# Kernel optimization log

Measured on AMD Instinct MI355X. Metric: run time of the kernel, lower is better.

The kernel has to match this reference:

```python
import jax, jax.numpy as jnp
import numpy as np

HEAD_SIZE = 64

def setup_inputs() -> dict:
    key = jax.random.key(0)
    k1, k2, k3, k4 = jax.random.split(key, 4)
    B, T, D = 4, 4096, 768
    x = jax.random.normal(k1, (B, T, D), dtype=jnp.float32)
    Wq = jax.random.normal(k2, (D, HEAD_SIZE), dtype=jnp.float32) * (1.0 / np.sqrt(D))
    Wk = jax.random.normal(k3, (D, HEAD_SIZE), dtype=jnp.float32) * (1.0 / np.sqrt(D))
    Wv = jax.random.normal(k4, (D, HEAD_SIZE), dtype=jnp.float32) * (1.0 / np.sqrt(D))
    return {"x": x, "Wq": Wq, "Wk": Wk, "Wv": Wv}

def reference(x, Wq, Wk, Wv):
    # q,k,v: [B, T, H]
    q = jnp.einsum('btd,dh->bth', x, Wq)
    k = jnp.einsum('btd,dh->bth', x, Wk)
    v = jnp.einsum('btd,dh->bth', x, Wv)
    # scores: [B, T, T]; causal mask via lower-triangular band, -inf elsewhere
    scores = jnp.einsum('bqh,bkh->bqk', q, k)
    T = x.shape[1]
    causal = jnp.tril(jnp.ones((T, T), dtype=bool))  # band_part(ones, -1, 0)
    scores = jnp.where(causal[None, :, :], scores, -jnp.inf)
    attn = jax.nn.softmax(scores / np.sqrt(HEAD_SIZE), axis=-1)
    # dropout is identity in eval mode
    return jnp.einsum('bqk,bkh->bqh', attn, v)
```

## Files before the change

kernel.cpp:

```cpp
#include <hip/hip_runtime.h>
#include <math.h>

typedef __attribute__((ext_vector_type(8))) short short8;
typedef __attribute__((ext_vector_type(4))) float f32x4;
typedef unsigned short ushort_t;

#define TSEQ   4096
#define NBATCH 4
#define DMODEL 768
#define HS     64
#define KSPLIT 4

static __device__ __forceinline__ ushort_t f2bf(float f) {
  union { float f; unsigned u; } v; v.f = f;
  unsigned r = v.u + 0x7fffu + ((v.u >> 16) & 1u);
  return (ushort_t)(r >> 16);
}
static __device__ __forceinline__ float bf2f(ushort_t u) {
  union { unsigned u; float f; } v; v.u = ((unsigned)u) << 16; return v.f;
}

#define MFMA16(a,b,c) __builtin_amdgcn_mfma_f32_16x16x32_bf16((a),(b),(c),0,0,0)

__global__ __launch_bounds__(256) void wprep(
    const float* __restrict__ Wq, const float* __restrict__ Wk,
    const float* __restrict__ Wv, ushort_t* __restrict__ Wt)
{
  __shared__ float lds[64 * 65];
  const int m = blockIdx.x / 12, kc = blockIdx.x % 12, k0 = kc * 64;
  const float* W = (m == 0) ? Wq : (m == 1) ? Wk : Wv;
  const int tid = threadIdx.x;
#pragma unroll
  for (int i = 0; i < 16; i++) {
    const int row = i * 4 + (tid >> 6), col = tid & 63;
    lds[row * 65 + col] = W[(size_t)(k0 + row) * HS + col];
  }
  __syncthreads();
#pragma unroll
  for (int i = 0; i < 16; i++) {
    const int n = i * 4 + (tid >> 6), kk = tid & 63;
    Wt[(size_t)(m * 64 + n) * DMODEL + k0 + kk] = f2bf(lds[kk * 65 + n]);
  }
}

#define XPITCH 772
__global__ __launch_bounds__(256, 3) void qkv_mfma(
    const float* __restrict__ x, const ushort_t* __restrict__ Wt,
    ushort_t* __restrict__ q, ushort_t* __restrict__ kO, ushort_t* __restrict__ vT)
{
  __shared__ __align__(16) float xp[16 * XPITCH];

  const int tid  = threadIdx.x;
  const int ns   = tid >> 6;
  const int lane = tid & 63;
  const int l16  = lane & 15, quad = lane >> 4;
  const int M0   = blockIdx.x * 16;

  {
    const int row0 = ns * 4;
#pragma unroll
    for (int r = 0; r < 4; r++) {
      const float* gsrc = x + (size_t)(M0 + row0 + r) * DMODEL;
      float*       ldst = xp + (row0 + r) * XPITCH;
#pragma unroll
      for (int c = 0; c < 3; c++) {
        __builtin_amdgcn_global_load_lds(
            (const __attribute__((address_space(1))) float*)(gsrc + c * 256 + lane * 4),
            (__attribute__((address_space(3))) float*)(ldst + c * 256),
            16, 0, 0);
      }
    }
  }

  const ushort_t* wb = Wt + (size_t)(ns * 48 + l16) * DMODEL + quad * 8;
  short8 bp[6];
#pragma unroll
  for (int nt = 0; nt < 3; nt++)
#pragma unroll
    for (int kc = 0; kc < 2; kc++)
      bp[nt * 2 + kc] = *(const short8*)(wb + (size_t)nt * 16 * DMODEL + kc * 32);

  f32x4 acc[3];
#pragma unroll
  for (int nt = 0; nt < 3; nt++) acc[nt] = (f32x4){0.f, 0.f, 0.f, 0.f};

  __syncthreads();

  for (int ks = 0; ks < DMODEL / 64; ks++) {
    short8 bc[6];
#pragma unroll
    for (int t = 0; t < 6; t++) bc[t] = bp[t];
    if (ks < DMODEL / 64 - 1) {
#pragma unroll
      for (int nt = 0; nt < 3; nt++)
#pragma unroll
        for (int kc = 0; kc < 2; kc++)
          bp[nt * 2 + kc] =
              *(const short8*)(wb + (size_t)nt * 16 * DMODEL + (ks + 1) * 64 + kc * 32);
    }
#pragma unroll
    for (int kc = 0; kc < 2; kc++) {
      const float* ar = xp + l16 * XPITCH + ks * 64 + kc * 32 + quad * 8;
      const float4 f0 = *(const float4*)(ar);
      const float4 f1 = *(const float4*)(ar + 4);
      short8 af;
      af[0] = f2bf(f0.x); af[1] = f2bf(f0.y); af[2] = f2bf(f0.z); af[3] = f2bf(f0.w);
      af[4] = f2bf(f1.x); af[5] = f2bf(f1.y); af[6] = f2bf(f1.z); af[7] = f2bf(f1.w);
#pragma unroll
      for (int nt = 0; nt < 3; nt++)
        acc[nt] = MFMA16(af, bc[nt * 2 + kc], acc[nt]);
    }
  }

#pragma unroll
  for (int nt = 0; nt < 3; nt++) {
    const int gnt = ns * 3 + nt;
    const int mat = gnt >> 2;
    const int col = (gnt & 3) * 16 + l16;
    if (mat == 0) {
#pragma unroll
      for (int r = 0; r < 4; r++)
        q[(size_t)(M0 + quad * 4 + r) * HS + col] = f2bf(acc[nt][r] * 0.125f);
    } else if (mat == 1) {
#pragma unroll
      for (int r = 0; r < 4; r++)
        kO[(size_t)(M0 + quad * 4 + r) * HS + col] = f2bf(acc[nt][r]);
    }
  }
  __syncthreads();
  float* vls = xp;
#pragma unroll
  for (int nt = 0; nt < 3; nt++) {
    const int gnt = ns * 3 + nt;
    if ((gnt >> 2) == 2) {
      const int col = (gnt & 3) * 16 + l16;
#pragma unroll
      for (int r = 0; r < 4; r++)
        vls[(quad * 4 + r) * 65 + col] = acc[nt][r];
    }
  }
  __syncthreads();
  if (tid < 128) {
    const int d = tid >> 1, seg = tid & 1;
    short8 pk;
#pragma unroll
    for (int i = 0; i < 8; i++) pk[i] = (short)f2bf(vls[(seg * 8 + i) * 65 + d]);
    *(short8*)(vT + ((size_t)(M0 >> 12) * HS + d) * TSEQ + (M0 & (TSEQ - 1)) + seg * 8) = pk;
  }
}

#define KP 72
__global__ __launch_bounds__(128) void attn_part(
    const ushort_t* __restrict__ q, const ushort_t* __restrict__ k,
    const ushort_t* __restrict__ vT, float* __restrict__ ML, ushort_t* __restrict__ OP)
{
  __shared__ __align__(16) ushort_t sK[64 * KP];
  __shared__ __align__(16) ushort_t sV[64 * KP];
  __shared__ __align__(16) ushort_t sP[2][16 * KP];

  const int idx  = blockIdx.x;
  const int s    = idx & 3;
  const int b    = (idx >> 2) & 3;
  const int jt   = 127 - (idx >> 4);
  const int tid  = threadIdx.x;
  const int w    = tid >> 6;
  const int lane = tid & 63;
  const int l16  = lane & 15, quad = lane >> 4;
  const int R0   = jt * 32 + w * 16;

  const ushort_t* qg = q  + (size_t)b * TSEQ * HS;
  const ushort_t* kg = k  + (size_t)b * TSEQ * HS;
  const ushort_t* vg = vT + (size_t)b * HS * TSEQ;

  const short8 qf0 = *(const short8*)(qg + (R0 + l16) * HS +      quad * 8);
  const short8 qf1 = *(const short8*)(qg + (R0 + l16) * HS + 32 + quad * 8);

  f32x4 o[4];
#pragma unroll
  for (int dt = 0; dt < 4; dt++) o[dt] = (f32x4){0.f, 0.f, 0.f, 0.f};
  float mrow = -INFINITY, lrow = 0.f;

  const int nkt = jt / 2 + 1;
  short8 kpre[4], vpre[4];
  int kt = s;
  if (kt < nkt) {
    const int k0 = kt * 64;
#pragma unroll
    for (int i = 0; i < 4; i++) {
      const int c = i * 128 + tid, key = c >> 3, ch = c & 7;
      kpre[i] = *(const short8*)(kg + (size_t)(k0 + key) * HS + ch * 8);
      vpre[i] = *(const short8*)(vg + (size_t)key * TSEQ + k0 + ch * 8);
    }
  }
  for (; kt < nkt; kt += KSPLIT) {
    const int k0 = kt * 64;
    __syncthreads();
#pragma unroll
    for (int i = 0; i < 4; i++) {
      const int c = i * 128 + tid, key = c >> 3, ch = c & 7;
      *(short8*)(sK + key * KP + ch * 8) = kpre[i];
      *(short8*)(sV + key * KP + ch * 8) = vpre[i];
    }
    if (kt + KSPLIT < nkt) {
      const int kn = (kt + KSPLIT) * 64;
#pragma unroll
      for (int i = 0; i < 4; i++) {
        const int c = i * 128 + tid, key = c >> 3, ch = c & 7;
        kpre[i] = *(const short8*)(kg + (size_t)(kn + key) * HS + ch * 8);
        vpre[i] = *(const short8*)(vg + (size_t)key * TSEQ + kn + ch * 8);
      }
    }
    __syncthreads();
    f32x4 sT[4];
#pragma unroll
    for (int ct = 0; ct < 4; ct++) {
      sT[ct] = (f32x4){0.f, 0.f, 0.f, 0.f};
      const short8 kfa = *(const short8*)(sK + (ct * 16 + l16) * KP +      quad * 8);
      const short8 kfb = *(const short8*)(sK + (ct * 16 + l16) * KP + 32 + quad * 8);
      sT[ct] = MFMA16(kfa, qf0, sT[ct]);
      sT[ct] = MFMA16(kfb, qf1, sT[ct]);
    }
    if (k0 + 63 > R0) {
      const int qrow = R0 + l16;
#pragma unroll
      for (int ct = 0; ct < 4; ct++)
#pragma unroll
        for (int r = 0; r < 4; r++)
          sT[ct][r] = (k0 + ct * 16 + quad * 4 + r <= qrow) ? sT[ct][r] : -INFINITY;
    }
    float tm = -INFINITY;
#pragma unroll
    for (int ct = 0; ct < 4; ct++)
#pragma unroll
      for (int r = 0; r < 4; r++) tm = fmaxf(tm, sT[ct][r]);
    tm = fmaxf(tm, __shfl_xor(tm, 16));
    tm = fmaxf(tm, __shfl_xor(tm, 32));
    const float mn = fmaxf(mrow, tm);
    const float al = __expf(mrow - mn);
    mrow = mn;
    float ps = 0.f;
#pragma unroll
    for (int ct = 0; ct < 4; ct++)
#pragma unroll
      for (int r = 0; r < 4; r++) { sT[ct][r] = __expf(sT[ct][r] - mn); ps += sT[ct][r]; }
    ps += __shfl_xor(ps, 16);
    ps += __shfl_xor(ps, 32);
    lrow = lrow * al + ps;
    ushort_t* Pw = &sP[w][0];
#pragma unroll
    for (int ct = 0; ct < 4; ct++) {
      ushort4 pk;
      pk.x = f2bf(sT[ct][0]); pk.y = f2bf(sT[ct][1]);
      pk.z = f2bf(sT[ct][2]); pk.w = f2bf(sT[ct][3]);
      *(ushort4*)(Pw + l16 * KP + ct * 16 + quad * 4) = pk;
    }
    float alo[4];
#pragma unroll
    for (int r = 0; r < 4; r++) alo[r] = __shfl(al, quad * 4 + r);
#pragma unroll
    for (int dt = 0; dt < 4; dt++)
#pragma unroll
      for (int r = 0; r < 4; r++) o[dt][r] *= alo[r];
    const short8 pf0 = *(const short8*)(Pw + l16 * KP +      quad * 8);
    const short8 pf1 = *(const short8*)(Pw + l16 * KP + 32 + quad * 8);
#pragma unroll
    for (int dt = 0; dt < 4; dt++) {
      const short8 vfa = *(const short8*)(sV + (dt * 16 + l16) * KP +      quad * 8);
      const short8 vfb = *(const short8*)(sV + (dt * 16 + l16) * KP + 32 + quad * 8);
      o[dt] = MFMA16(pf0, vfa, o[dt]);
      o[dt] = MFMA16(pf1, vfb, o[dt]);
    }
  }

  const size_t base = ((size_t)(b * KSPLIT + s) * TSEQ);
  if (quad == 0) {
    ML[(base + R0 + l16) * 2 + 0] = mrow;
    ML[(base + R0 + l16) * 2 + 1] = lrow;
  }
#pragma unroll
  for (int dt = 0; dt < 4; dt++)
#pragma unroll
    for (int r = 0; r < 4; r++)
      OP[(base + R0 + quad * 4 + r) * HS + dt * 16 + l16] = f2bf(o[dt][r]);
}

__global__ __launch_bounds__(256) void attn_merge(
    const float* __restrict__ ML, const ushort_t* __restrict__ OP,
    float* __restrict__ out)
{
  const int row = blockIdx.x * 16 + (threadIdx.x >> 4);
  const int b   = row >> 12, t = row & (TSEQ - 1);
  const int d0  = (threadIdx.x & 15) * 4;
  float m[KSPLIT], l[KSPLIT];
  float M = -INFINITY;
#pragma unroll
  for (int ss = 0; ss < KSPLIT; ss++) {
    const size_t i = ((size_t)(b * KSPLIT + ss) * TSEQ + t);
    m[ss] = ML[i * 2]; l[ss] = ML[i * 2 + 1];
    M = fmaxf(M, m[ss]);
  }
  float den = 0.f;
  float4 num = make_float4(0.f, 0.f, 0.f, 0.f);
#pragma unroll
  for (int ss = 0; ss < KSPLIT; ss++) {
    const float a = __expf(m[ss] - M);
    den += l[ss] * a;
    const size_t i = ((size_t)(b * KSPLIT + ss) * TSEQ + t);
    const ushort4 u = *(const ushort4*)(OP + i * HS + d0);
    num.x += a * bf2f(u.x); num.y += a * bf2f(u.y);
    num.z += a * bf2f(u.z); num.w += a * bf2f(u.w);
  }
  const float inv = 1.f / den;
  *(float4*)(out + (size_t)row * HS + d0) =
      make_float4(num.x * inv, num.y * inv, num.z * inv, num.w * inv);
}

extern "C" void kernel_launch(void* const* d_in, const int* in_sizes, int n_in,
                              void* d_out, int out_size, void* d_ws, size_t ws_size,
                              hipStream_t stream) {
  const float* x  = (const float*)d_in[0];
  const float* Wq = (const float*)d_in[1];
  const float* Wk = (const float*)d_in[2];
  const float* Wv = (const float*)d_in[3];
  float* out = (float*)d_out;

  char* ws = (char*)d_ws;
  ushort_t* Wt = (ushort_t*)ws;
  ushort_t* qb = (ushort_t*)(ws + 294912);
  ushort_t* kb = (ushort_t*)(ws + 294912 + 2097152);
  ushort_t* vb = (ushort_t*)(ws + 294912 + 2 * 2097152);
  float*    ml = (float*)   (ws + 294912 + 3 * 2097152);
  ushort_t* op = (ushort_t*)(ws + 294912 + 3 * 2097152 + 524288);

  wprep<<<36, 256, 0, stream>>>(Wq, Wk, Wv, Wt);
  qkv_mfma<<<(NBATCH * TSEQ) / 16, 256, 0, stream>>>(x, Wt, qb, kb, vb);
  attn_part<<<128 * NBATCH * KSPLIT, 128, 0, stream>>>(qb, kb, vb, ml, op);
  attn_merge<<<1024, 256, 0, stream>>>(ml, op, out);
}
```

Baseline: 151.9 us.

## Restructure QKV projection with 32-row tiles and double-buffered LDS staging

Measured after the change: 131.1 us. 13.7% less time.

```diff
diff --git a/kernel.cpp b/kernel.cpp
--- a/kernel.cpp
+++ b/kernel.cpp
@@ -43,110 +43,131 @@
   }
 }
 
-#define XPITCH 772
-__global__ __launch_bounds__(256, 3) void qkv_mfma(
+__global__ __launch_bounds__(256, 2) void qkv_mfma(
     const float* __restrict__ x, const ushort_t* __restrict__ Wt,
     ushort_t* __restrict__ q, ushort_t* __restrict__ kO, ushort_t* __restrict__ vT)
 {
-  __shared__ __align__(16) float xp[16 * XPITCH];
+  __shared__ __align__(16) ushort_t sA[2][32 * 72];
+  __shared__ __align__(16) ushort_t sB[2][192 * 64];
 
   const int tid  = threadIdx.x;
-  const int ns   = tid >> 6;
+  const int w    = tid >> 6;
   const int lane = tid & 63;
   const int l16  = lane & 15, quad = lane >> 4;
-  const int M0   = blockIdx.x * 16;
+  const int M0   = blockIdx.x * 32;
+
+  const int arow = tid >> 3, acol = (tid & 7) * 8;
+  const float* ax = x + (size_t)(M0 + arow) * DMODEL + acol;
+
+  const int bcol_l = lane >> 3;
+  const int bkoff  = (((lane & 7) ^ (bcol_l & 7)) << 3);
+
+  f32x4 acc[2][3];
+#pragma unroll
+  for (int mt = 0; mt < 2; mt++)
+#pragma unroll
+    for (int nt = 0; nt < 3; nt++) acc[mt][nt] = (f32x4){0.f, 0.f, 0.f, 0.f};
 
   {
-    const int row0 = ns * 4;
-#pragma unroll
-    for (int r = 0; r < 4; r++) {
-      const float* gsrc = x + (size_t)(M0 + row0 + r) * DMODEL;
-      float*       ldst = xp + (row0 + r) * XPITCH;
-#pragma unroll
-      for (int c = 0; c < 3; c++) {
+#pragma unroll
+    for (int j = 0; j < 6; j++) {
+      const int colb = w * 48 + j * 8;
+      __builtin_amdgcn_global_load_lds(
+          (const __attribute__((address_space(1))) ushort_t*)
+              (Wt + (size_t)(colb + bcol_l) * DMODEL + bkoff),
+          (__attribute__((address_space(3))) ushort_t*)(&sB[0][colb * 64]),
+          16, 0, 0);
+    }
+    const float4 f0 = *(const float4*)(ax);
+    const float4 f1 = *(const float4*)(ax + 4);
+    short8 p;
+    p[0]=f2bf(f0.x); p[1]=f2bf(f0.y); p[2]=f2bf(f0.z); p[3]=f2bf(f0.w);
+    p[4]=f2bf(f1.x); p[5]=f2bf(f1.y); p[6]=f2bf(f1.z); p[7]=f2bf(f1.w);
+    *(short8*)(&sA[0][arow * 72 + acol]) = p;
+  }
+
+  for (int ks = 0; ks < DMODEL / 64; ks++) {
+    const int cur = ks & 1, nxt = cur ^ 1;
+    __syncthreads();
+
+    float4 f0n, f1n;
+    if (ks < DMODEL / 64 - 1) {
+#pragma unroll
+      for (int j = 0; j < 6; j++) {
+        const int colb = w * 48 + j * 8;
         __builtin_amdgcn_global_load_lds(
-            (const __attribute__((address_space(1))) float*)(gsrc + c * 256 + lane * 4),
-            (__attribute__((address_space(3))) float*)(ldst + c * 256),
+            (const __attribute__((address_space(1))) ushort_t*)
+                (Wt + (size_t)(colb + bcol_l) * DMODEL + (ks + 1) * 64 + bkoff),
+            (__attribute__((address_space(3))) ushort_t*)(&sB[nxt][colb * 64]),
             16, 0, 0);
       }
-    }
-  }
-
-  const ushort_t* wb = Wt + (size_t)(ns * 48 + l16) * DMODEL + quad * 8;
-  short8 bp[6];
-#pragma unroll
-  for (int nt = 0; nt < 3; nt++)
-#pragma unroll
-    for (int kc = 0; kc < 2; kc++)
-      bp[nt * 2 + kc] = *(const short8*)(wb + (size_t)nt * 16 * DMODEL + kc * 32);
-
-  f32x4 acc[3];
-#pragma unroll
-  for (int nt = 0; nt < 3; nt++) acc[nt] = (f32x4){0.f, 0.f, 0.f, 0.f};
-
+      f0n = *(const float4*)(ax + (ks + 1) * 64);
+      f1n = *(const float4*)(ax + (ks + 1) * 64 + 4);
+    }
+
+    const ushort_t* sAc = &sA[cur][0];
+    const ushort_t* sBc = &sB[cur][0];
+#pragma unroll
+    for (int kc = 0; kc < 2; kc++) {
+      const short8 a0 = *(const short8*)(sAc + (l16)      * 72 + kc * 32 + quad * 8);
+      const short8 a1 = *(const short8*)(sAc + (16 + l16) * 72 + kc * 32 + quad * 8);
+      const int kswz = (kc * 32 + quad * 8) ^ ((l16 & 7) << 3);
+#pragma unroll
+      for (int nt = 0; nt < 3; nt++) {
+        const short8 bf =
+            *(const short8*)(sBc + (w * 48 + nt * 16 + l16) * 64 + kswz);
+        acc[0][nt] = MFMA16(a0, bf, acc[0][nt]);
+        acc[1][nt] = MFMA16(a1, bf, acc[1][nt]);
+      }
+    }
+
+    if (ks < DMODEL / 64 - 1) {
+      short8 p;
+      p[0]=f2bf(f0n.x); p[1]=f2bf(f0n.y); p[2]=f2bf(f0n.z); p[3]=f2bf(f0n.w);
+      p[4]=f2bf(f1n.x); p[5]=f2bf(f1n.y); p[6]=f2bf(f1n.z); p[7]=f2bf(f1n.w);
+      *(short8*)(&sA[nxt][arow * 72 + acol]) = p;
+    }
+  }
+
+#pragma unroll
+  for (int mt = 0; mt < 2; mt++)
+#pragma unroll
+    for (int nt = 0; nt < 3; nt++) {
+      const int gnt = w * 3 + nt;
+      const int mat = gnt >> 2;
+      const int col = (gnt & 3) * 16 + l16;
+      if (mat == 0) {
+#pragma unroll
+        for (int r = 0; r < 4; r++)
+          q[(size_t)(M0 + mt * 16 + quad * 4 + r) * HS + col] =
+              f2bf(acc[mt][nt][r] * 0.125f);
+      } else if (mat == 1) {
+#pragma unroll
+        for (int r = 0; r < 4; r++)
+          kO[(size_t)(M0 + mt * 16 + quad * 4 + r) * HS + col] =
+              f2bf(acc[mt][nt][r]);
+      }
+    }
   __syncthreads();
-
-  for (int ks = 0; ks < DMODEL / 64; ks++) {
-    short8 bc[6];
-#pragma unroll
-    for (int t = 0; t < 6; t++) bc[t] = bp[t];
-    if (ks < DMODEL / 64 - 1) {
-#pragma unroll
-      for (int nt = 0; nt < 3; nt++)
-#pragma unroll
-        for (int kc = 0; kc < 2; kc++)
-          bp[nt * 2 + kc] =
-              *(const short8*)(wb + (size_t)nt * 16 * DMODEL + (ks + 1) * 64 + kc * 32);
-    }
-#pragma unroll
-    for (int kc = 0; kc < 2; kc++) {
-      const float* ar = xp + l16 * XPITCH + ks * 64 + kc * 32 + quad * 8;
-      const float4 f0 = *(const float4*)(ar);
-      const float4 f1 = *(const float4*)(ar + 4);
-      short8 af;
-      af[0] = f2bf(f0.x); af[1] = f2bf(f0.y); af[2] = f2bf(f0.z); af[3] = f2bf(f0.w);
-      af[4] = f2bf(f1.x); af[5] = f2bf(f1.y); af[6] = f2bf(f1.z); af[7] = f2bf(f1.w);
-#pragma unroll
-      for (int nt = 0; nt < 3; nt++)
-        acc[nt] = MFMA16(af, bc[nt * 2 + kc], acc[nt]);
-    }
-  }
-
-#pragma unroll
-  for (int nt = 0; nt < 3; nt++) {
-    const int gnt = ns * 3 + nt;
-    const int mat = gnt >> 2;
-    const int col = (gnt & 3) * 16 + l16;
-    if (mat == 0) {
-#pragma unroll
-      for (int r = 0; r < 4; r++)
-        q[(size_t)(M0 + quad * 4 + r) * HS + col] = f2bf(acc[nt][r] * 0.125f);
-    } else if (mat == 1) {
-#pragma unroll
-      for (int r = 0; r < 4; r++)
-        kO[(size_t)(M0 + quad * 4 + r) * HS + col] = f2bf(acc[nt][r]);
-    }
-  }
+  float* vls = (float*)&sA[0][0];
+#pragma unroll
+  for (int mt = 0; mt < 2; mt++)
+#pragma unroll
+    for (int nt = 0; nt < 3; nt++) {
+      const int gnt = w * 3 + nt;
+      if ((gnt >> 2) == 2) {
+        const int vcol = (gnt & 3) * 16 + l16;
+#pragma unroll
+        for (int r = 0; r < 4; r++)
+          vls[(mt * 16 + quad * 4 + r) * 65 + vcol] = acc[mt][nt][r];
+      }
+    }
   __syncthreads();
-  float* vls = xp;
-#pragma unroll
-  for (int nt = 0; nt < 3; nt++) {
-    const int gnt = ns * 3 + nt;
-    if ((gnt >> 2) == 2) {
-      const int col = (gnt & 3) * 16 + l16;
-#pragma unroll
-      for (int r = 0; r < 4; r++)
-        vls[(quad * 4 + r) * 65 + col] = acc[nt][r];
-    }
-  }
-  __syncthreads();
-  if (tid < 128) {
-    const int d = tid >> 1, seg = tid & 1;
-    short8 pk;
-#pragma unroll
-    for (int i = 0; i < 8; i++) pk[i] = (short)f2bf(vls[(seg * 8 + i) * 65 + d]);
-    *(short8*)(vT + ((size_t)(M0 >> 12) * HS + d) * TSEQ + (M0 & (TSEQ - 1)) + seg * 8) = pk;
-  }
+  const int d = tid >> 2, seg = tid & 3;
+  short8 pk;
+#pragma unroll
+  for (int i = 0; i < 8; i++) pk[i] = (short)f2bf(vls[(seg * 8 + i) * 65 + d]);
+  *(short8*)(vT + ((size_t)(M0 >> 12) * HS + d) * TSEQ + (M0 & (TSEQ - 1)) + seg * 8) = pk;
 }
 
 #define KP 72
@@ -333,7 +354,7 @@
   ushort_t* op = (ushort_t*)(ws + 294912 + 3 * 2097152 + 524288);
 
   wprep<<<36, 256, 0, stream>>>(Wq, Wk, Wv, Wt);
-  qkv_mfma<<<(NBATCH * TSEQ) / 16, 256, 0, stream>>>(x, Wt, qb, kb, vb);
+  qkv_mfma<<<(NBATCH * TSEQ) / 32, 256, 0, stream>>>(x, Wt, qb, kb, vb);
   attn_part<<<128 * NBATCH * KSPLIT, 128, 0, stream>>>(qb, kb, vb, ml, op);
   attn_merge<<<1024, 256, 0, stream>>>(ml, op, out);
 }
```
